# Kernel tuning notes

Measured on AMD Instinct MI355X. Metric: run time of the kernel, lower is better.

The kernel has to match this reference:

```python
import jax, jax.numpy as jnp
import numpy as np

TOPK = 8
NUM_EXPERTS = 64


def setup_inputs() -> dict:
    key = jax.random.key(0)
    k0, k1, k2, k3 = jax.random.split(key, 4)
    B, S, H, E = 4, 4096, 2048, NUM_EXPERTS
    scale = (2.0 ** -0.5) * np.sqrt(6.0 / (H + E))  # xavier_uniform gain 2^-0.5
    return {
        "x": jax.random.normal(k0, (B, S, H), dtype=jnp.float32),
        "w_transform": jax.random.uniform(k1, (E, H), jnp.float32, -scale, scale),
        "w_noise": jax.random.uniform(k2, (E, H), jnp.float32, -scale, scale),
        "noise": jax.random.normal(k3, (E,), dtype=jnp.float32),
    }


def reference(x, w_transform, w_noise, noise):
    # weight: [B, S, E]
    logits_t = jnp.einsum("bsh,eh->bse", x, w_transform)
    logits_n = jnp.einsum("bsh,eh->bse", x, w_noise)
    weight = logits_t + jax.nn.softplus(logits_n) * noise  # broadcast noise [E]

    # Global (corpus-level) top-k over expert means
    mean_w = weight.mean(axis=(0, 1))  # [E]
    gates, indexes = jax.lax.top_k(mean_w, TOPK)
    selected_gates = jax.nn.softmax(gates, axis=-1)  # [TOPK]

    # Example-wise top-k -> multi-hot mask [B, S, E]
    _, ew_idx = jax.lax.top_k(weight, TOPK)  # [B, S, TOPK]
    mask = jax.nn.one_hot(ew_idx, NUM_EXPERTS, dtype=weight.dtype).sum(axis=-2) > 0

    # Masked softmax over experts
    masked = jnp.where(mask, weight, -jnp.inf)
    soft_w = jax.nn.softmax(masked, axis=-1)  # [B, S, E]

    # Experts balance loss: (std / mean)^2 of per-expert total weight
    sum_w = soft_w.sum(axis=(0, 1))  # [E]
    cv = jnp.std(sum_w, ddof=1) / jnp.mean(sum_w)  # torch .std() is unbiased
    balance_loss = cv ** 2

    return selected_gates, indexes, balance_loss
```

## Files before the change

kernel.cpp:

```cpp
#include <hip/hip_runtime.h>
#include <math.h>

#define H     2048
#define NE    64
#define KTOP  8
#define NTOK  16384

typedef __attribute__((ext_vector_type(8))) __bf16 bf16x8;
typedef __attribute__((ext_vector_type(8))) unsigned short us8;
typedef __attribute__((ext_vector_type(4))) float f32x4;

__device__ __forceinline__ unsigned short f2bf(float f) {
    unsigned u = __builtin_bit_cast(unsigned, f);
    return (unsigned short)((u + 0x7FFFu + ((u >> 16) & 1u)) >> 16);
}

__global__ __launch_bounds__(256) void k_prep(const float* __restrict__ Wt,
                                              const float* __restrict__ Wn,
                                              unsigned short* __restrict__ wbf2,
                                              float* __restrict__ sums) {
    const int gid = blockIdx.x * 256 + threadIdx.x;
    if (blockIdx.x == 0 && threadIdx.x < 128) sums[threadIdx.x] = 0.f;

    const int ln  = gid & 63;
    const int nb  = (gid >> 6) & 7;
    const int k32 = gid >> 9;
    const int row = nb * 16 + (ln & 15);
    const int col = k32 * 32 + (ln >> 4) * 8;
    const float* src = (row < NE) ? (Wt + (size_t)row * H + col)
                                  : (Wn + (size_t)(row - NE) * H + col);
    float4 v0 = *(const float4*)src;
    float4 v1 = *(const float4*)(src + 4);
    us8 o;
    o[0] = f2bf(v0.x); o[1] = f2bf(v0.y); o[2] = f2bf(v0.z); o[3] = f2bf(v0.w);
    o[4] = f2bf(v1.x); o[5] = f2bf(v1.y); o[6] = f2bf(v1.z); o[7] = f2bf(v1.w);
    *(us8*)(wbf2 + (size_t)gid * 8) = o;
}

__global__ __launch_bounds__(256, 3) void k_main(const float* __restrict__ X,
                                                 const unsigned short* __restrict__ wbf2,
                                                 const float* __restrict__ noise,
                                                 float* __restrict__ sumraw,
                                                 float* __restrict__ sumsoft) {
    __shared__ float cb[3][2048];
    __shared__ float ep[16][68];
    __shared__ float lsoft[NE];

    const int tid  = threadIdx.x;
    const int wid  = tid >> 6;
    const int lane = tid & 63;
    const int lr   = lane & 15;
    const int lg   = lane >> 4;
    const int t0   = blockIdx.x * 16;

    if (wid == 1) lsoft[lane] = 0.f;

    const float* xp = X + (size_t)(t0 + lr) * H + wid * 512 + lg * 8;
    const unsigned short* wp = wbf2 + (size_t)wid * 16 * 4096 + (size_t)lane * 8;

    f32x4 acc[8];
    #pragma unroll
    for (int i = 0; i < 8; ++i) acc[i] = (f32x4){0.f, 0.f, 0.f, 0.f};

    bf16x8 bb[2][8];
    float4 xa[2][2];

    #pragma unroll
    for (int nb = 0; nb < 8; ++nb)
        bb[0][nb] = *(const bf16x8*)(wp + (size_t)nb * 512);
    xa[0][0] = *(const float4*)(xp);
    xa[0][1] = *(const float4*)(xp + 4);
    xa[1][0] = *(const float4*)(xp + 32);
    xa[1][1] = *(const float4*)(xp + 36);

    #pragma unroll
    for (int p = 0; p < 16; ++p) {
        const int cu = p & 1;
        const int nx = cu ^ 1;
        if (p < 15) {
            const unsigned short* bp = wp + (size_t)(p + 1) * 4096;
            #pragma unroll
            for (int nb = 0; nb < 8; ++nb)
                bb[nx][nb] = *(const bf16x8*)(bp + (size_t)nb * 512);
        }
        float4 c0 = xa[cu][0], c1 = xa[cu][1];
        bf16x8 af;
        af[0] = (__bf16)c0.x; af[1] = (__bf16)c0.y;
        af[2] = (__bf16)c0.z; af[3] = (__bf16)c0.w;
        af[4] = (__bf16)c1.x; af[5] = (__bf16)c1.y;
        af[6] = (__bf16)c1.z; af[7] = (__bf16)c1.w;
        if (p + 2 < 16) {
            xa[cu][0] = *(const float4*)(xp + (p + 2) * 32);
            xa[cu][1] = *(const float4*)(xp + (p + 2) * 32 + 4);
        }
        #pragma unroll
        for (int nb = 0; nb < 8; ++nb)
            acc[nb] = __builtin_amdgcn_mfma_f32_16x16x32_bf16(af, bb[cu][nb], acc[nb], 0, 0, 0);
    }

    if (wid > 0) {
        #pragma unroll
        for (int nb = 0; nb < 8; ++nb)
            #pragma unroll
            for (int r = 0; r < 4; ++r)
                cb[wid - 1][(nb * 4 + r) * 64 + lane] = acc[nb][r];
    }
    __syncthreads();

    if (wid == 0) {
        #pragma unroll
        for (int nb = 0; nb < 8; ++nb)
            #pragma unroll
            for (int r = 0; r < 4; ++r) {
                int idx = (nb * 4 + r) * 64 + lane;
                acc[nb][r] += cb[0][idx] + cb[1][idx] + cb[2][idx];
            }
        float nz[4];
        #pragma unroll
        for (int nb = 0; nb < 4; ++nb) nz[nb] = noise[nb * 16 + lr];
        #pragma unroll
        for (int nb = 0; nb < 4; ++nb)
            #pragma unroll
            for (int r = 0; r < 4; ++r) {
                float lt  = acc[nb][r];
                float lnv = acc[nb + 4][r];
                float sp  = fmaxf(lnv, 0.f) + log1pf(expf(-fabsf(lnv)));
                ep[lg * 4 + r][nb * 16 + lr] = lt + sp * nz[nb];
            }
    }
    __syncthreads();

    if (wid == 0 && lane < 16) {
        float tv[KTOP]; int ti[KTOP];
        #pragma unroll
        for (int q = 0; q < KTOP; ++q) { tv[q] = -INFINITY; ti[q] = 0; }
        for (int e = 0; e < NE; ++e) {
            float cv = ep[lane][e]; int ci = e;
            #pragma unroll
            for (int q = 0; q < KTOP; ++q) {
                if (cv > tv[q]) {
                    float t_ = tv[q]; int i_ = ti[q];
                    tv[q] = cv; ti[q] = ci;
                    cv = t_; ci = i_;
                }
            }
        }
        float m = tv[0], den = 0.f, pr[KTOP];
        #pragma unroll
        for (int q = 0; q < KTOP; ++q) { pr[q] = expf(tv[q] - m); den += pr[q]; }
        float inv = 1.f / den;
        #pragma unroll
        for (int q = 0; q < KTOP; ++q) atomicAdd(&lsoft[ti[q]], pr[q] * inv);
    }
    if (wid == 1) {
        float s = 0.f;
        #pragma unroll
        for (int t = 0; t < 16; ++t) s += ep[t][lane];
        atomicAdd(&sumraw[lane], s);
    }
    __syncthreads();
    if (wid == 2) atomicAdd(&sumsoft[lane], lsoft[lane]);
}

__global__ void k_final(const float* __restrict__ sumraw,
                        const float* __restrict__ sumsoft,
                        float* __restrict__ out) {
    if (threadIdx.x != 0 || blockIdx.x != 0) return;

    float mw[NE];
    for (int e = 0; e < NE; ++e) mw[e] = sumraw[e] * (1.f / (float)NTOK);

    float tv[KTOP]; int ti[KTOP];
    for (int q = 0; q < KTOP; ++q) { tv[q] = -INFINITY; ti[q] = 0; }
    for (int e = 0; e < NE; ++e) {
        float cv = mw[e]; int ci = e;
        for (int q = 0; q < KTOP; ++q) {
            if (cv > tv[q]) {
                float t_ = tv[q]; int i_ = ti[q];
                tv[q] = cv; ti[q] = ci;
                cv = t_; ci = i_;
            }
        }
    }
    float m = tv[0], den = 0.f, pr[KTOP];
    for (int q = 0; q < KTOP; ++q) { pr[q] = expf(tv[q] - m); den += pr[q]; }
    for (int q = 0; q < KTOP; ++q) {
        out[q] = pr[q] / den;
        out[KTOP + q] = (float)ti[q];
    }

    float s = 0.f;
    for (int e = 0; e < NE; ++e) s += sumsoft[e];
    float mean = s / (float)NE;
    float var = 0.f;
    for (int e = 0; e < NE; ++e) { float d = sumsoft[e] - mean; var += d * d; }
    var /= (float)(NE - 1);
    out[16] = var / (mean * mean);
}

extern "C" void kernel_launch(void* const* d_in, const int* in_sizes, int n_in,
                              void* d_out, int out_size, void* d_ws, size_t ws_size,
                              hipStream_t stream) {
    (void)in_sizes; (void)n_in; (void)out_size; (void)ws_size;
    const float* x     = (const float*)d_in[0];
    const float* wt    = (const float*)d_in[1];
    const float* wn    = (const float*)d_in[2];
    const float* noise = (const float*)d_in[3];
    float* out = (float*)d_out;

    float* sumraw  = (float*)d_ws;
    float* sumsoft = sumraw + NE;
    unsigned short* wbf2 = (unsigned short*)(sumsoft + NE);

    k_prep<<<128, 256, 0, stream>>>(wt, wn, wbf2, sumraw);
    k_main<<<1024, 256, 0, stream>>>(x, wbf2, noise, sumraw, sumsoft);
    k_final<<<1, 64, 0, stream>>>(sumraw, sumsoft, out);
}
```

Measured before the change: 110.6 us.

## Use 64-token blocks with 2-way K split and triple-buffered asm loads

Each block now handles 64 tokens with 8 waves (4 token groups by 2 K-halves) instead of 16 tokens with 4 K-split waves. The grid shrinks to 256 blocks of 512 threads. Global loads go through inline asm with explicit vmcnt waits across a three-slot prefetch ring, which deepens memory latency hiding for the bandwidth-bound stream of X. The top-k and softmax epilogue runs on 64 threads per block and global atomics drop fourfold. The cost is higher register and LDS pressure, and with 256 blocks on many CUs occupancy and tail balance may suffer.

```diff
diff --git a/kernel.cpp b/kernel.cpp
--- a/kernel.cpp
+++ b/kernel.cpp
@@ -5,6 +5,8 @@
 #define NE    64
 #define KTOP  8
 #define NTOK  16384
+#define TOKB  64
+#define STEPS 32
 
 typedef __attribute__((ext_vector_type(8))) __bf16 bf16x8;
 typedef __attribute__((ext_vector_type(8))) unsigned short us8;
@@ -14,6 +16,13 @@
     unsigned u = __builtin_bit_cast(unsigned, f);
     return (unsigned short)((u + 0x7FFFu + ((u >> 16) & 1u)) >> 16);
 }
+
+#define GLOAD_F4(dst, ptr, OFF)                                        \
+    asm volatile("global_load_dwordx4 %0, %1, off offset:%2"           \
+                 : "=v"(dst) : "v"(ptr), "i"(OFF))
+#define WAITV(N)                                                       \
+    do { asm volatile("s_waitcnt vmcnt(%0)" :: "i"(N));                \
+         __builtin_amdgcn_sched_barrier(0); } while (0)
 
 __global__ __launch_bounds__(256) void k_prep(const float* __restrict__ Wt,
                                               const float* __restrict__ Wn,
@@ -37,84 +46,94 @@
     *(us8*)(wbf2 + (size_t)gid * 8) = o;
 }
 
-__global__ __launch_bounds__(256, 3) void k_main(const float* __restrict__ X,
+__global__ __launch_bounds__(512, 2) void k_main(const float* __restrict__ X,
                                                  const unsigned short* __restrict__ wbf2,
                                                  const float* __restrict__ noise,
                                                  float* __restrict__ sumraw,
                                                  float* __restrict__ sumsoft) {
-    __shared__ float cb[3][2048];
-    __shared__ float ep[16][68];
+    __shared__ float cb[4][2048];
+    __shared__ float epf[TOKB * 68];
     __shared__ float lsoft[NE];
 
     const int tid  = threadIdx.x;
     const int wid  = tid >> 6;
     const int lane = tid & 63;
+    const int wm   = wid & 3;
+    const int kp   = wid >> 2;
     const int lr   = lane & 15;
     const int lg   = lane >> 4;
-    const int t0   = blockIdx.x * 16;
-
-    if (wid == 1) lsoft[lane] = 0.f;
-
-    const float* xp = X + (size_t)(t0 + lr) * H + wid * 512 + lg * 8;
-    const unsigned short* wp = wbf2 + (size_t)wid * 16 * 4096 + (size_t)lane * 8;
+    const int t0   = blockIdx.x * TOKB;
+
+    if (tid < NE) lsoft[tid] = 0.f;
+
+    const float* xp = X + (size_t)(t0 + wm * 16 + lr) * H + kp * 1024 + lg * 8;
+    const unsigned short* bp0 = wbf2 + (size_t)kp * 32 * 4096 + (size_t)lane * 8;
 
     f32x4 acc[8];
     #pragma unroll
     for (int i = 0; i < 8; ++i) acc[i] = (f32x4){0.f, 0.f, 0.f, 0.f};
 
-    bf16x8 bb[2][8];
-    float4 xa[2][2];
+    float4 xb[3][2];
+    us8    bb[3][8];
+
+    #define ISSUE(slot, s)                                                   \
+        do {                                                                 \
+            const unsigned short* bA = bp0 + (size_t)(s) * 4096;             \
+            const unsigned short* bB = bA + 2048;                            \
+            GLOAD_F4(bb[slot][0], bA, 0);                                    \
+            GLOAD_F4(bb[slot][1], bA, 1024);                                 \
+            GLOAD_F4(bb[slot][2], bA, 2048);                                 \
+            GLOAD_F4(bb[slot][3], bA, 3072);                                 \
+            GLOAD_F4(bb[slot][4], bB, 0);                                    \
+            GLOAD_F4(bb[slot][5], bB, 1024);                                 \
+            GLOAD_F4(bb[slot][6], bB, 2048);                                 \
+            GLOAD_F4(bb[slot][7], bB, 3072);                                 \
+            const float* xA = xp + (s) * 32;                                 \
+            GLOAD_F4(xb[slot][0], xA, 0);                                    \
+            GLOAD_F4(xb[slot][1], xA, 16);                                   \
+        } while (0)
+
+    ISSUE(0, 0);
+    ISSUE(1, 1);
+    ISSUE(2, 2);
 
     #pragma unroll
-    for (int nb = 0; nb < 8; ++nb)
-        bb[0][nb] = *(const bf16x8*)(wp + (size_t)nb * 512);
-    xa[0][0] = *(const float4*)(xp);
-    xa[0][1] = *(const float4*)(xp + 4);
-    xa[1][0] = *(const float4*)(xp + 32);
-    xa[1][1] = *(const float4*)(xp + 36);
-
-    #pragma unroll
-    for (int p = 0; p < 16; ++p) {
-        const int cu = p & 1;
-        const int nx = cu ^ 1;
-        if (p < 15) {
-            const unsigned short* bp = wp + (size_t)(p + 1) * 4096;
-            #pragma unroll
-            for (int nb = 0; nb < 8; ++nb)
-                bb[nx][nb] = *(const bf16x8*)(bp + (size_t)nb * 512);
-        }
-        float4 c0 = xa[cu][0], c1 = xa[cu][1];
+    for (int j = 0; j < STEPS; ++j) {
+        const int slot = j % 3;
+        if (j < STEPS - 2)      WAITV(20);
+        else if (j == STEPS - 2) WAITV(10);
+        else                     WAITV(0);
+
+        float4 c0 = xb[slot][0], c1 = xb[slot][1];
         bf16x8 af;
         af[0] = (__bf16)c0.x; af[1] = (__bf16)c0.y;
         af[2] = (__bf16)c0.z; af[3] = (__bf16)c0.w;
         af[4] = (__bf16)c1.x; af[5] = (__bf16)c1.y;
         af[6] = (__bf16)c1.z; af[7] = (__bf16)c1.w;
-        if (p + 2 < 16) {
-            xa[cu][0] = *(const float4*)(xp + (p + 2) * 32);
-            xa[cu][1] = *(const float4*)(xp + (p + 2) * 32 + 4);
+        #pragma unroll
+        for (int nb = 0; nb < 8; ++nb) {
+            bf16x8 bfr = __builtin_bit_cast(bf16x8, bb[slot][nb]);
+            acc[nb] = __builtin_amdgcn_mfma_f32_16x16x32_bf16(af, bfr, acc[nb], 0, 0, 0);
         }
+        if (j + 3 < STEPS) ISSUE(slot, j + 3);
+    }
+    #undef ISSUE
+
+    if (kp == 1) {
         #pragma unroll
         for (int nb = 0; nb < 8; ++nb)
-            acc[nb] = __builtin_amdgcn_mfma_f32_16x16x32_bf16(af, bb[cu][nb], acc[nb], 0, 0, 0);
-    }
-
-    if (wid > 0) {
+            #pragma unroll
+            for (int r = 0; r < 4; ++r)
+                cb[wm][(nb * 4 + r) * 64 + lane] = acc[nb][r];
+    }
+    __syncthreads();
+
+    if (kp == 0) {
         #pragma unroll
         for (int nb = 0; nb < 8; ++nb)
             #pragma unroll
             for (int r = 0; r < 4; ++r)
-                cb[wid - 1][(nb * 4 + r) * 64 + lane] = acc[nb][r];
-    }
-    __syncthreads();
-
-    if (wid == 0) {
-        #pragma unroll
-        for (int nb = 0; nb < 8; ++nb)
-            #pragma unroll
-            for (int r = 0; r < 4; ++r) {
-                int idx = (nb * 4 + r) * 64 + lane;
-                acc[nb][r] += cb[0][idx] + cb[1][idx] + cb[2][idx];
-            }
+                acc[nb][r] += cb[wm][(nb * 4 + r) * 64 + lane];
         float nz[4];
         #pragma unroll
         for (int nb = 0; nb < 4; ++nb) nz[nb] = noise[nb * 16 + lr];
@@ -125,17 +144,17 @@
                 float lt  = acc[nb][r];
                 float lnv = acc[nb + 4][r];
                 float sp  = fmaxf(lnv, 0.f) + log1pf(expf(-fabsf(lnv)));
-                ep[lg * 4 + r][nb * 16 + lr] = lt + sp * nz[nb];
+                epf[(wm * 16 + lg * 4 + r) * 68 + nb * 16 + lr] = lt + sp * nz[nb];
             }
     }
     __syncthreads();
 
-    if (wid == 0 && lane < 16) {
+    if (tid < TOKB) {
         float tv[KTOP]; int ti[KTOP];
         #pragma unroll
         for (int q = 0; q < KTOP; ++q) { tv[q] = -INFINITY; ti[q] = 0; }
         for (int e = 0; e < NE; ++e) {
-            float cv = ep[lane][e]; int ci = e;
+            float cv = epf[tid * 68 + e]; int ci = e;
             #pragma unroll
             for (int q = 0; q < KTOP; ++q) {
                 if (cv > tv[q]) {
@@ -152,14 +171,15 @@
         #pragma unroll
         for (int q = 0; q < KTOP; ++q) atomicAdd(&lsoft[ti[q]], pr[q] * inv);
     }
-    if (wid == 1) {
+    __syncthreads();
+
+    if (tid < NE) {
         float s = 0.f;
         #pragma unroll
-        for (int t = 0; t < 16; ++t) s += ep[t][lane];
-        atomicAdd(&sumraw[lane], s);
-    }
-    __syncthreads();
-    if (wid == 2) atomicAdd(&sumsoft[lane], lsoft[lane]);
+        for (int t = 0; t < TOKB; ++t) s += epf[t * 68 + tid];
+        atomicAdd(&sumraw[tid], s);
+        atomicAdd(&sumsoft[tid], lsoft[tid]);
+    }
 }
 
 __global__ void k_final(const float* __restrict__ sumraw,
@@ -213,6 +233,6 @@
     unsigned short* wbf2 = (unsigned short*)(sumsoft + NE);
 
     k_prep<<<128, 256, 0, stream>>>(wt, wn, wbf2, sumraw);
-    k_main<<<1024, 256, 0, stream>>>(x, wbf2, noise, sumraw, sumsoft);
+    k_main<<<256, 512, 0, stream>>>(x, wbf2, noise, sumraw, sumsoft);
     k_final<<<1, 64, 0, stream>>>(sumraw, sumsoft, out);
 }
```

Measured after the change: 94.12 us. -14.9%, faster.
